# Kernel tuning notes

Hardware: AMD Instinct MI355X
Metric: run time of the kernel (lower is better)

The kernel has to match this reference:

```python
import jax, jax.numpy as jnp
import numpy as np

N_NODES = 100000


def gcn_conv(x, src, dst, W, b, n_nodes):
    # PyG GCNConv: h = W^T x, then symmetric-normalized aggregation over (A + I), then + b
    h = x @ W  # [N, out]
    ones = jnp.ones(src.shape[0], dtype=h.dtype)
    deg = jax.ops.segment_sum(ones, dst, num_segments=n_nodes)  # in-degree incl. self-loops
    dinv = jnp.where(deg > 0, jax.lax.rsqrt(deg), 0.0)
    norm = dinv[src] * dinv[dst]  # [E]
    msg = h[src] * norm[:, None]  # gather + scale  [E, out]
    out = jax.ops.segment_sum(msg, dst, num_segments=n_nodes)  # scatter-add  [N, out]
    return out + b


def setup_inputs() -> dict:
    key = jax.random.key(0)
    k = jax.random.split(key, 8)
    num_features, hidden = 128, 32
    n_edges = 3_200_000
    x = jax.random.normal(k[0], (N_NODES, num_features), dtype=jnp.float32)
    edge_index = jax.random.randint(k[1], (2, n_edges), 0, N_NODES, dtype=jnp.int64)
    def glorot(kk, shape):
        fan_in, fan_out = shape
        s = (6.0 / (fan_in + fan_out)) ** 0.5
        return jax.random.uniform(kk, shape, jnp.float32, -s, s)
    return {
        "x": x,
        "edge_index": edge_index,
        "W1": glorot(k[2], (num_features, hidden)),
        "b1": jnp.zeros((hidden,), jnp.float32),
        "W2": glorot(k[3], (hidden, hidden)),
        "b2": jnp.zeros((hidden,), jnp.float32),
        "Wfc": glorot(k[4], (hidden, 1)),
        "bfc": jnp.zeros((1,), jnp.float32),
    }


def reference(x, edge_index, W1, b1, W2, b2, Wfc, bfc):
    n = x.shape[0]
    # add self-loops (GCNConv default add_self_loops=True)
    loops = jnp.arange(n, dtype=edge_index.dtype)
    src = jnp.concatenate([edge_index[0], loops])
    dst = jnp.concatenate([edge_index[1], loops])
    h = jax.nn.relu(gcn_conv(x, src, dst, W1, b1, n))
    # F.dropout with training=False (eval) is identity
    h = jax.nn.relu(gcn_conv(h, src, dst, W2, b2, n))
    scores = (h @ Wfc + bfc).squeeze(-1)  # [N]
    return scores
```

## Files before the change

kernel.cpp:

```cpp
#include <hip/hip_runtime.h>


constexpr int NN  = 100000;
constexpr int FIN = 128;
constexpr int H   = 32;
constexpr int SCAN_B = 1024;
constexpr int SCAN_NB = (NN + SCAN_B - 1) / SCAN_B;

__global__ void zero_int_kernel(int* __restrict__ p, int n) {
  int i = blockIdx.x * blockDim.x + threadIdx.x;
  if (i < n) p[i] = 0;
}

__global__ void hist_kernel(const int* __restrict__ dst, int* __restrict__ cnt, int E) {
  int stride = gridDim.x * blockDim.x;
  for (int e = blockIdx.x * blockDim.x + threadIdx.x; e < E; e += stride)
    atomicAdd(&cnt[dst[e]], 1);
}

__global__ void scan1_kernel(const int* __restrict__ cnt, int* __restrict__ row_start,
                             int* __restrict__ blksum, int n) {
  __shared__ int sm[2][SCAN_B];
  int tid = threadIdx.x;
  int i = blockIdx.x * SCAN_B + tid;
  int v = (i < n) ? cnt[i] : 0;
  sm[0][tid] = v;
  __syncthreads();
  int cur = 0;
  #pragma unroll
  for (int off = 1; off < SCAN_B; off <<= 1) {
    int a = sm[cur][tid];
    if (tid >= off) a += sm[cur][tid - off];
    sm[cur ^ 1][tid] = a;
    cur ^= 1;
    __syncthreads();
  }
  if (i < n) row_start[i] = sm[cur][tid] - v;
  if (tid == SCAN_B - 1) blksum[blockIdx.x] = sm[cur][tid];
}

__global__ void scan2_kernel(int* __restrict__ blksum, int nb) {
  if (threadIdx.x == 0 && blockIdx.x == 0) {
    int run = 0;
    for (int b = 0; b < nb; ++b) { int t = blksum[b]; blksum[b] = run; run += t; }
  }
}

__global__ void scan3_kernel(int* __restrict__ row_start, const int* __restrict__ blksum,
                             const int* __restrict__ cnt, float* __restrict__ dinv, int n) {
  int i = blockIdx.x * blockDim.x + threadIdx.x;
  if (i >= n) return;
  row_start[i] += blksum[i / SCAN_B];
  dinv[i] = rsqrtf((float)cnt[i] + 1.0f);
}

__global__ void fill_kernel(const int* __restrict__ src, const int* __restrict__ dst,
                            int* __restrict__ row_start, int* __restrict__ csr, int E) {
  int stride = gridDim.x * blockDim.x;
  for (int e = blockIdx.x * blockDim.x + threadIdx.x; e < E; e += stride) {
    int pos = atomicAdd(&row_start[dst[e]], 1);
    csr[pos] = src[e];
  }
}

__global__ void gemm1_kernel(const float* __restrict__ x, const float* __restrict__ W,
                             float* __restrict__ h, int n) {
  __shared__ float Wl[FIN * H];
  for (int t = threadIdx.x; t < FIN * H; t += blockDim.x) Wl[t] = W[t];
  __syncthreads();
  int t = blockIdx.x * blockDim.x + threadIdx.x;
  int i = t >> 5, j = t & 31;
  if (i >= n) return;
  const float4* xr = (const float4*)(x + (size_t)i * FIN);
  float acc = 0.f;
  #pragma unroll 8
  for (int k4 = 0; k4 < FIN / 4; ++k4) {
    float4 v = xr[k4];
    acc += v.x * Wl[(k4 * 4 + 0) * H + j];
    acc += v.y * Wl[(k4 * 4 + 1) * H + j];
    acc += v.z * Wl[(k4 * 4 + 2) * H + j];
    acc += v.w * Wl[(k4 * 4 + 3) * H + j];
  }
  h[t] = acc;
}

__global__ void gemm2_kernel(const float* __restrict__ a, const float* __restrict__ W,
                             float* __restrict__ h, int n) {
  __shared__ float Wl[H * H];
  for (int t = threadIdx.x; t < H * H; t += blockDim.x) Wl[t] = W[t];
  __syncthreads();
  int t = blockIdx.x * blockDim.x + threadIdx.x;
  int i = t >> 5, j = t & 31;
  if (i >= n) return;
  const float4* ar = (const float4*)(a + (size_t)i * H);
  float acc = 0.f;
  #pragma unroll
  for (int k4 = 0; k4 < H / 4; ++k4) {
    float4 v = ar[k4];
    acc += v.x * Wl[(k4 * 4 + 0) * H + j];
    acc += v.y * Wl[(k4 * 4 + 1) * H + j];
    acc += v.z * Wl[(k4 * 4 + 2) * H + j];
    acc += v.w * Wl[(k4 * 4 + 3) * H + j];
  }
  h[t] = acc;
}

__global__ void gather1_kernel(const int* __restrict__ csr, const int* __restrict__ cnt,
                               const int* __restrict__ rend, const float* __restrict__ dinv,
                               const float* __restrict__ h, const float* __restrict__ b,
                               float* __restrict__ a1, int n) {
  int t = blockIdx.x * blockDim.x + threadIdx.x;
  int r = t >> 5, j = t & 31;
  if (r >= n) return;
  int end = rend[r];
  int k = end - cnt[r];
  float acc = 0.f;
  for (; k + 4 <= end; k += 4) {
    int s0 = csr[k], s1 = csr[k + 1], s2 = csr[k + 2], s3 = csr[k + 3];
    float v0 = h[s0 * H + j], v1 = h[s1 * H + j], v2 = h[s2 * H + j], v3 = h[s3 * H + j];
    acc += v0 * dinv[s0]; acc += v1 * dinv[s1];
    acc += v2 * dinv[s2]; acc += v3 * dinv[s3];
  }
  for (; k < end; ++k) { int s = csr[k]; acc += h[s * H + j] * dinv[s]; }
  float di = dinv[r];
  float v = acc * di + h[t] * di * di + b[j];
  a1[t] = fmaxf(v, 0.f);
}

__global__ void gather2_kernel(const int* __restrict__ csr, const int* __restrict__ cnt,
                               const int* __restrict__ rend, const float* __restrict__ dinv,
                               const float* __restrict__ h2, const float* __restrict__ b2,
                               const float* __restrict__ Wfc, const float* __restrict__ bfc,
                               float* __restrict__ out, int n) {
  int t = blockIdx.x * blockDim.x + threadIdx.x;
  int r = t >> 5, j = t & 31;
  if (r >= n) return;
  int end = rend[r];
  int k = end - cnt[r];
  float acc = 0.f;
  for (; k + 4 <= end; k += 4) {
    int s0 = csr[k], s1 = csr[k + 1], s2 = csr[k + 2], s3 = csr[k + 3];
    float v0 = h2[s0 * H + j], v1 = h2[s1 * H + j], v2 = h2[s2 * H + j], v3 = h2[s3 * H + j];
    acc += v0 * dinv[s0]; acc += v1 * dinv[s1];
    acc += v2 * dinv[s2]; acc += v3 * dinv[s3];
  }
  for (; k < end; ++k) { int s = csr[k]; acc += h2[s * H + j] * dinv[s]; }
  float di = dinv[r];
  float v = acc * di + h2[t] * di * di + b2[j];
  v = fmaxf(v, 0.f) * Wfc[j];
  #pragma unroll
  for (int m = 16; m; m >>= 1) v += __shfl_xor(v, m, 32);
  if (j == 0) out[r] = v + bfc[0];
}

extern "C" void kernel_launch(void* const* d_in, const int* in_sizes, int n_in,
                              void* d_out, int out_size, void* d_ws, size_t ws_size,
                              hipStream_t stream) {
  const float* x   = (const float*)d_in[0];
  const int*   ei  = (const int*)d_in[1];
  const float* W1  = (const float*)d_in[2];
  const float* b1  = (const float*)d_in[3];
  const float* W2  = (const float*)d_in[4];
  const float* b2  = (const float*)d_in[5];
  const float* Wfc = (const float*)d_in[6];
  const float* bfc = (const float*)d_in[7];
  float* out = (float*)d_out;

  const int E = in_sizes[1] / 2;
  const int* src = ei;
  const int* dst = ei + E;

  char* w = (char*)d_ws;
  int*   csr       = (int*)w;                    w += (size_t)E * 4;
  int*   cnt       = (int*)w;                    w += (size_t)NN * 4;
  int*   row_start = (int*)w;                    w += (size_t)NN * 4;
  float* dinv      = (float*)w;                  w += (size_t)NN * 4;
  float* h         = (float*)w;                  w += (size_t)NN * H * 4;
  float* a1        = (float*)w;
  int*   blksum    = (int*)a1;

  const int nb_nh = (NN * H + 255) / 256;
  const int nb_n  = (NN + 255) / 256;

  zero_int_kernel<<<nb_n, 256, 0, stream>>>(cnt, NN);
  hist_kernel<<<2048, 256, 0, stream>>>(dst, cnt, E);
  scan1_kernel<<<SCAN_NB, SCAN_B, 0, stream>>>(cnt, row_start, blksum, NN);
  scan2_kernel<<<1, 64, 0, stream>>>(blksum, SCAN_NB);
  scan3_kernel<<<nb_n, 256, 0, stream>>>(row_start, blksum, cnt, dinv, NN);
  fill_kernel<<<2048, 256, 0, stream>>>(src, dst, row_start, csr, E);
  gemm1_kernel<<<nb_nh, 256, 0, stream>>>(x, W1, h, NN);
  gather1_kernel<<<nb_nh, 256, 0, stream>>>(csr, cnt, row_start, dinv, h, b1, a1, NN);
  gemm2_kernel<<<nb_nh, 256, 0, stream>>>(a1, W2, h, NN);
  gather2_kernel<<<nb_nh, 256, 0, stream>>>(csr, cnt, row_start, dinv, h, b2, Wfc, bfc, out, NN);
}
```

Baseline: 769.7 us.

## Build CSR via two-level bucket sort with block-local per-row binning

Replaces the global per-node histogram, three-stage scan and global-atomic fill with a two-level counting sort. Edges are first binned into 128-row buckets using few global atomics, staged as (src,dst) pairs. A per-bucket kernel then computes row counts, offsets and dinv, and scatters sources into the CSR with shared-memory atomics. The gathers now read row starts rather than row ends. The aim is to cut global atomic contention and scattered writes, at the cost of an extra staging pass that aliases the h buffer and uses the output buffer as scratch.

```diff
diff --git a/kernel.cpp b/kernel.cpp
--- a/kernel.cpp
+++ b/kernel.cpp
@@ -4,62 +4,95 @@
 constexpr int NN  = 100000;
 constexpr int FIN = 128;
 constexpr int H   = 32;
-constexpr int SCAN_B = 1024;
-constexpr int SCAN_NB = (NN + SCAN_B - 1) / SCAN_B;
-
-__global__ void zero_int_kernel(int* __restrict__ p, int n) {
-  int i = blockIdx.x * blockDim.x + threadIdx.x;
+constexpr int BSH = 7;
+constexpr int BRW = 1 << BSH;
+constexpr int NB  = (NN + BRW - 1) >> BSH;
+
+__global__ void zero_small_kernel(int* __restrict__ p, int n) {
+  int i = threadIdx.x;
   if (i < n) p[i] = 0;
 }
 
-__global__ void hist_kernel(const int* __restrict__ dst, int* __restrict__ cnt, int E) {
+__global__ void bucket_hist_kernel(const int* __restrict__ dst, int* __restrict__ bkcnt, int E) {
   int stride = gridDim.x * blockDim.x;
   for (int e = blockIdx.x * blockDim.x + threadIdx.x; e < E; e += stride)
-    atomicAdd(&cnt[dst[e]], 1);
-}
-
-__global__ void scan1_kernel(const int* __restrict__ cnt, int* __restrict__ row_start,
-                             int* __restrict__ blksum, int n) {
-  __shared__ int sm[2][SCAN_B];
+    atomicAdd(&bkcnt[dst[e] >> BSH], 1);
+}
+
+__global__ void bucket_scan_kernel(const int* __restrict__ bkcnt, int* __restrict__ bkcur, int nb) {
+  __shared__ int sm[2][1024];
   int tid = threadIdx.x;
-  int i = blockIdx.x * SCAN_B + tid;
-  int v = (i < n) ? cnt[i] : 0;
+  int v = (tid < nb) ? bkcnt[tid] : 0;
   sm[0][tid] = v;
   __syncthreads();
   int cur = 0;
   #pragma unroll
-  for (int off = 1; off < SCAN_B; off <<= 1) {
+  for (int off = 1; off < 1024; off <<= 1) {
     int a = sm[cur][tid];
     if (tid >= off) a += sm[cur][tid - off];
     sm[cur ^ 1][tid] = a;
     cur ^= 1;
     __syncthreads();
   }
-  if (i < n) row_start[i] = sm[cur][tid] - v;
-  if (tid == SCAN_B - 1) blksum[blockIdx.x] = sm[cur][tid];
-}
-
-__global__ void scan2_kernel(int* __restrict__ blksum, int nb) {
-  if (threadIdx.x == 0 && blockIdx.x == 0) {
-    int run = 0;
-    for (int b = 0; b < nb; ++b) { int t = blksum[b]; blksum[b] = run; run += t; }
-  }
-}
-
-__global__ void scan3_kernel(int* __restrict__ row_start, const int* __restrict__ blksum,
-                             const int* __restrict__ cnt, float* __restrict__ dinv, int n) {
-  int i = blockIdx.x * blockDim.x + threadIdx.x;
-  if (i >= n) return;
-  row_start[i] += blksum[i / SCAN_B];
-  dinv[i] = rsqrtf((float)cnt[i] + 1.0f);
-}
-
-__global__ void fill_kernel(const int* __restrict__ src, const int* __restrict__ dst,
-                            int* __restrict__ row_start, int* __restrict__ csr, int E) {
+  if (tid < nb) bkcur[tid] = sm[cur][tid] - v;
+}
+
+__global__ void bin_kernel(const int* __restrict__ src, const int* __restrict__ dst,
+                           int* __restrict__ bkcur, int2* __restrict__ tmp, int E) {
   int stride = gridDim.x * blockDim.x;
-  for (int e = blockIdx.x * blockDim.x + threadIdx.x; e < E; e += stride) {
-    int pos = atomicAdd(&row_start[dst[e]], 1);
-    csr[pos] = src[e];
+  for (int e = blockIdx.x * blockDim.x + threadIdx.x; e += 0, e < E; e += stride) {
+    int d = dst[e];
+    int pos = atomicAdd(&bkcur[d >> BSH], 1);
+    tmp[pos] = make_int2(src[e], d);
+  }
+}
+
+__global__ void finalize_kernel(const int2* __restrict__ tmp, const int* __restrict__ bkcur,
+                                int* __restrict__ cnt, int* __restrict__ row_start,
+                                float* __restrict__ dinv, int* __restrict__ csr, int n) {
+  __shared__ int lcnt[BRW];
+  __shared__ int lscan[2][BRW];
+  __shared__ int lcur[BRW];
+  int b = blockIdx.x;
+  int tid = threadIdx.x;
+  int t0 = b ? bkcur[b - 1] : 0;
+  int t1 = bkcur[b];
+  int r0 = b << BSH;
+  int nr = min(BRW, n - r0);
+
+  if (tid < BRW) lcnt[tid] = 0;
+  __syncthreads();
+  for (int e = t0 + tid; e < t1; e += blockDim.x)
+    atomicAdd(&lcnt[tmp[e].y - r0], 1);
+  __syncthreads();
+
+  int cur = 0;
+  if (tid < BRW) lscan[0][tid] = lcnt[tid];
+  __syncthreads();
+  #pragma unroll
+  for (int off = 1; off < BRW; off <<= 1) {
+    if (tid < BRW) {
+      int a = lscan[cur][tid];
+      if (tid >= off) a += lscan[cur][tid - off];
+      lscan[cur ^ 1][tid] = a;
+    }
+    cur ^= 1;
+    __syncthreads();
+  }
+  if (tid < nr) {
+    int c = lcnt[tid];
+    int start = t0 + lscan[cur][tid] - c;
+    cnt[r0 + tid] = c;
+    row_start[r0 + tid] = start;
+    dinv[r0 + tid] = rsqrtf((float)c + 1.0f);
+    lcur[tid] = start;
+  }
+  __syncthreads();
+
+  for (int e = t0 + tid; e < t1; e += blockDim.x) {
+    int2 p = tmp[e];
+    int pos = atomicAdd(&lcur[p.y - r0], 1);
+    csr[pos] = p.x;
   }
 }
 
@@ -106,14 +139,14 @@
 }
 
 __global__ void gather1_kernel(const int* __restrict__ csr, const int* __restrict__ cnt,
-                               const int* __restrict__ rend, const float* __restrict__ dinv,
+                               const int* __restrict__ rstart, const float* __restrict__ dinv,
                                const float* __restrict__ h, const float* __restrict__ b,
                                float* __restrict__ a1, int n) {
   int t = blockIdx.x * blockDim.x + threadIdx.x;
   int r = t >> 5, j = t & 31;
   if (r >= n) return;
-  int end = rend[r];
-  int k = end - cnt[r];
+  int k = rstart[r];
+  int end = k + cnt[r];
   float acc = 0.f;
   for (; k + 4 <= end; k += 4) {
     int s0 = csr[k], s1 = csr[k + 1], s2 = csr[k + 2], s3 = csr[k + 3];
@@ -128,15 +161,15 @@
 }
 
 __global__ void gather2_kernel(const int* __restrict__ csr, const int* __restrict__ cnt,
-                               const int* __restrict__ rend, const float* __restrict__ dinv,
+                               const int* __restrict__ rstart, const float* __restrict__ dinv,
                                const float* __restrict__ h2, const float* __restrict__ b2,
                                const float* __restrict__ Wfc, const float* __restrict__ bfc,
                                float* __restrict__ out, int n) {
   int t = blockIdx.x * blockDim.x + threadIdx.x;
   int r = t >> 5, j = t & 31;
   if (r >= n) return;
-  int end = rend[r];
-  int k = end - cnt[r];
+  int k = rstart[r];
+  int end = k + cnt[r];
   float acc = 0.f;
   for (; k + 4 <= end; k += 4) {
     int s0 = csr[k], s1 = csr[k + 1], s2 = csr[k + 2], s3 = csr[k + 3];
@@ -175,19 +208,20 @@
   int*   cnt       = (int*)w;                    w += (size_t)NN * 4;
   int*   row_start = (int*)w;                    w += (size_t)NN * 4;
   float* dinv      = (float*)w;                  w += (size_t)NN * 4;
-  float* h         = (float*)w;                  w += (size_t)NN * H * 4;
-  float* a1        = (float*)w;
-  int*   blksum    = (int*)a1;
+  float* h         = (float*)w;
+  int2*  tmp       = (int2*)h;
+  float* a1        = h + (size_t)NN * H;
+
+  int* bkcnt = (int*)d_out;
+  int* bkcur = (int*)d_out + 1024;
 
   const int nb_nh = (NN * H + 255) / 256;
-  const int nb_n  = (NN + 255) / 256;
-
-  zero_int_kernel<<<nb_n, 256, 0, stream>>>(cnt, NN);
-  hist_kernel<<<2048, 256, 0, stream>>>(dst, cnt, E);
-  scan1_kernel<<<SCAN_NB, SCAN_B, 0, stream>>>(cnt, row_start, blksum, NN);
-  scan2_kernel<<<1, 64, 0, stream>>>(blksum, SCAN_NB);
-  scan3_kernel<<<nb_n, 256, 0, stream>>>(row_start, blksum, cnt, dinv, NN);
-  fill_kernel<<<2048, 256, 0, stream>>>(src, dst, row_start, csr, E);
+
+  zero_small_kernel<<<1, 1024, 0, stream>>>(bkcnt, NB);
+  bucket_hist_kernel<<<2048, 256, 0, stream>>>(dst, bkcnt, E);
+  bucket_scan_kernel<<<1, 1024, 0, stream>>>(bkcnt, bkcur, NB);
+  bin_kernel<<<2048, 256, 0, stream>>>(src, dst, bkcur, tmp, E);
+  finalize_kernel<<<NB, 256, 0, stream>>>(tmp, bkcur, cnt, row_start, dinv, csr, NN);
   gemm1_kernel<<<nb_nh, 256, 0, stream>>>(x, W1, h, NN);
   gather1_kernel<<<nb_nh, 256, 0, stream>>>(csr, cnt, row_start, dinv, h, b1, a1, NN);
   gemm2_kernel<<<nb_nh, 256, 0, stream>>>(a1, W2, h, NN);
```

Result: slower. 1.866 ms (+142.5%).
